# Performance work log

Measured on AMD Instinct MI355X. Metric: run time of the kernel, lower is better.

## Reference

```python
import jax, jax.numpy as jnp
import numpy as np

NEG_INF = -1e30

def mask_logits(target, mask):
    return target * mask + (1.0 - mask) * NEG_INF

def setup_inputs() -> dict:
    key = jax.random.key(0)
    k1, k2, k3 = jax.random.split(key, 3)
    B, D, Lc, Lq = 32, 256, 2048, 256
    C = jax.random.normal(k1, (B, D, Lc), dtype=jnp.float32)
    Q = jax.random.normal(k2, (B, D, Lq), dtype=jnp.float32)
    cmask = jnp.ones((B, Lc), dtype=jnp.float32)
    qmask = jnp.ones((B, Lq), dtype=jnp.float32)
    lim = np.sqrt(1.0 / D)
    w = jax.random.uniform(k3, (3 * D,), dtype=jnp.float32, minval=-lim, maxval=lim)
    return {"C": C, "Q": Q, "cmask": cmask, "qmask": qmask, "w": w}

def reference(C, Q, cmask, qmask, w):
    # C: (B, D, Lc), Q: (B, D, Lq) -> transpose to (B, L, D)
    Ct = jnp.swapaxes(C, 1, 2)            # (B, Lc, D)
    Qt = jnp.swapaxes(Q, 1, 2)            # (B, Lq, D)
    D = Ct.shape[-1]
    w1, w2, w3 = w[:D], w[D:2 * D], w[2 * D:]
    # S[b,c,q] = Ct[b,c]@w1 + Qt[b,q]@w2 + (Ct[b,c]*w3)@Qt[b,q]
    # (identical to matmul(cat([Ct,Qt,Ct*Qt],-1), w) without the 4-D tensor)
    S = (Ct @ w1)[:, :, None] + (Qt @ w2)[:, None, :] \
        + jnp.einsum('bcd,bqd->bcq', Ct * w3, Qt)     # (B, Lc, Lq)
    qm = qmask[:, None, :]                 # (B, 1, Lq)
    cm = cmask[:, :, None]                 # (B, Lc, 1)
    S1 = jax.nn.softmax(mask_logits(S, qm), axis=2)   # over query dim
    S2 = jax.nn.softmax(mask_logits(S, cm), axis=1)   # over context dim
    A = jnp.einsum('bcq,bqd->bcd', S1, Qt)            # (B, Lc, D)
    Bv = jnp.einsum('bck,bkd->bcd',
                    jnp.einsum('bcq,bkq->bck', S1, S2), Ct)  # (B, Lc, D)
    out = jnp.concatenate([Ct, A, Ct * A, Ct * Bv], axis=2)  # (B, Lc, 4D)
    # dropout omitted (eval mode)
    return jnp.swapaxes(out, 1, 2)         # (B, 4D, Lc)
```

## Files before the change

### kernel.cpp

```cpp
#include <hip/hip_runtime.h>


#define B_ 32
#define D_ 256
#define LC 2048
#define LQ 256
#define KSPLIT 4
#define NEG_INF (-1e30f)

using bf16   = __bf16;
using bf16x4 = __attribute__((ext_vector_type(4))) __bf16;
using bf16x8 = __attribute__((ext_vector_type(8))) __bf16;
using f32x4  = __attribute__((ext_vector_type(4))) float;

static __device__ __forceinline__ f32x4 mfma16(bf16x8 a, bf16x8 b, f32x4 c) {
  return __builtin_amdgcn_mfma_f32_16x16x32_bf16(a, b, c, 0, 0, 0);
}
static __device__ __forceinline__ void nt_store4(float* p, f32x4 v) {
  __builtin_nontemporal_store(v, (f32x4*)p);
}

__global__ __launch_bounds__(256) void qprep(const float* __restrict__ Q,
                                             const float* __restrict__ w,
                                             bf16* __restrict__ Qtb,
                                             bf16* __restrict__ Qb16,
                                             float* __restrict__ bqp) {
  __shared__ float t[64][65];
  __shared__ float pb[4][64];
  const int b  = blockIdx.y;
  const int qt = (blockIdx.x >> 2) * 64;
  const int dtI = blockIdx.x & 3, dt = dtI * 64;
  const int c  = threadIdx.x & 63, r0 = threadIdx.x >> 6;
  const float* Qb = Q + (size_t)b * D_ * LQ;
  bf16* Qcb = Qb16 + (size_t)b * D_ * LQ;
  float partial = 0.f;
#pragma unroll
  for (int r = r0; r < 64; r += 4) {
    const float v = Qb[(size_t)(dt + r) * LQ + qt + c];
    t[r][c] = v;
    Qcb[(size_t)(dt + r) * LQ + qt + c] = (bf16)v;
    partial += v * w[D_ + dt + r];
  }
  pb[r0][c] = partial;
  __syncthreads();
  bf16* O = Qtb + (size_t)b * LQ * D_;
#pragma unroll
  for (int r = r0; r < 64; r += 4)
    O[(size_t)(qt + r) * D_ + dt + c] = (bf16)t[c][r];
  if (r0 == 0)
    bqp[((size_t)(b * 4 + dtI)) * LQ + qt + c] = pb[0][c] + pb[1][c] + pb[2][c] + pb[3][c];
}

__global__ __launch_bounds__(256) void k1_sgemm(
    const float* __restrict__ C, const bf16* __restrict__ Qtb,
    const float* __restrict__ w, const float* __restrict__ cmask,
    const float* __restrict__ qmask, const float* __restrict__ bqp,
    bf16* __restrict__ S1, bf16* __restrict__ S1t,
    float* __restrict__ cpmax, float* __restrict__ cpsum) {
  __shared__ union __align__(16) SmU {
    struct { bf16 As[64][72]; bf16 Bs[256][72]; } st;
    bf16 tb[256][72];
    bf16 sb[64][264];
  } smu;
  __shared__ float ared[4][64];
  __shared__ float wred[4][64];
  __shared__ float wsum[4][64];
  __shared__ float cml[64];
  __shared__ float qml[256];
  __shared__ float bql[256];

  const int b = blockIdx.y, ct = blockIdx.x, c0 = ct * 64;
  const int tid = threadIdx.x, lane = tid & 63, wv = tid >> 6;
  const float* Cb = C + (size_t)b * D_ * LC;
  const bf16* Qt = Qtb + (size_t)b * LQ * D_;
  const float* w1 = w;
  const float* w3 = w + 2 * D_;

  if (tid < 64) cml[tid] = cmask[b * LC + c0 + tid];
  qml[tid] = qmask[b * LQ + tid];
  bql[tid] = bqp[(size_t)(b * 4 + 0) * LQ + tid] + bqp[(size_t)(b * 4 + 1) * LQ + tid] +
             bqp[(size_t)(b * 4 + 2) * LQ + tid] + bqp[(size_t)(b * 4 + 3) * LQ + tid];

  f32x4 acc[4][4];
#pragma unroll
  for (int i = 0; i < 4; i++)
#pragma unroll
    for (int j = 0; j < 4; j++) acc[i][j] = {0.f, 0.f, 0.f, 0.f};
  float acc_a = 0.f;

  const int sm = tid & 63;
  const int skg = tid >> 6;

  float aPre[16];
  bf16x8 bPre[8];
#pragma unroll
  for (int i = 0; i < 16; ++i)
    aPre[i] = Cb[(size_t)(skg * 16 + i) * LC + c0 + sm];
#pragma unroll
  for (int p = 0; p < 8; ++p) {
    const int idx = (p * 256 + tid) * 8;
    bPre[p] = *(const bf16x8*)(Qt + (size_t)(idx >> 6) * D_ + (idx & 63));
  }

  for (int it = 0; it < 4; ++it) {
    const int k0 = it * 64;
#pragma unroll
    for (int i = 0; i < 16; ++i) {
      const int k = skg * 16 + i, kgl = k0 + k;
      smu.st.As[sm][k] = (bf16)(aPre[i] * w3[kgl]);
      acc_a += aPre[i] * w1[kgl];
    }
#pragma unroll
    for (int p = 0; p < 8; ++p) {
      const int idx = (p * 256 + tid) * 8;
      *(bf16x8*)(&smu.st.Bs[idx >> 6][idx & 63]) = bPre[p];
    }
    __syncthreads();
    if (it < 3) {
#pragma unroll
      for (int i = 0; i < 16; ++i)
        aPre[i] = Cb[(size_t)(k0 + 64 + skg * 16 + i) * LC + c0 + sm];
#pragma unroll
      for (int p = 0; p < 8; ++p) {
        const int idx = (p * 256 + tid) * 8;
        bPre[p] = *(const bf16x8*)(Qt + (size_t)(idx >> 6) * D_ + k0 + 64 + (idx & 63));
      }
    }
#pragma unroll
    for (int kk = 0; kk < 64; kk += 32) {
      bf16x8 af[4], bfr[4];
#pragma unroll
      for (int mi = 0; mi < 4; mi++)
        af[mi] = *(const bf16x8*)(&smu.st.As[mi * 16 + (lane & 15)][kk + (lane >> 4) * 8]);
#pragma unroll
      for (int ni = 0; ni < 4; ni++)
        bfr[ni] = *(const bf16x8*)(&smu.st.Bs[wv * 64 + ni * 16 + (lane & 15)][kk + (lane >> 4) * 8]);
#pragma unroll
      for (int mi = 0; mi < 4; mi++)
#pragma unroll
        for (int ni = 0; ni < 4; ni++)
          acc[mi][ni] = mfma16(af[mi], bfr[ni], acc[mi][ni]);
    }
    __syncthreads();
  }

  ared[skg][sm] = acc_a;
  __syncthreads();

  const int r4 = (lane >> 4) * 4;
  const int cn = lane & 15;

#pragma unroll
  for (int mi = 0; mi < 4; mi++)
#pragma unroll
    for (int j = 0; j < 4; j++) {
      const int m = mi * 16 + r4 + j;
      const float aval = ared[0][m] + ared[1][m] + ared[2][m] + ared[3][m];
#pragma unroll
      for (int ni = 0; ni < 4; ni++) {
        const int n = wv * 64 + ni * 16 + cn;
        const bf16 sb = (bf16)(acc[mi][ni][j] + aval + bql[n]);
        acc[mi][ni][j] = (float)sb;
      }
    }

#pragma unroll
  for (int ni = 0; ni < 4; ni++) {
    const int n = wv * 64 + ni * 16 + cn;
    float mx = -3.0e38f;
#pragma unroll
    for (int mi = 0; mi < 4; mi++)
#pragma unroll
      for (int j = 0; j < 4; j++) {
        const int m = mi * 16 + r4 + j;
        const float cmv = cml[m];
        const float lg = acc[mi][ni][j] * cmv + (1.f - cmv) * NEG_INF;
        mx = fmaxf(mx, lg);
      }
    mx = fmaxf(mx, __shfl_xor(mx, 16));
    mx = fmaxf(mx, __shfl_xor(mx, 32));
    float ps = 0.f;
#pragma unroll
    for (int mi = 0; mi < 4; mi++)
#pragma unroll
      for (int j = 0; j < 4; j++) {
        const int m = mi * 16 + r4 + j;
        const float cmv = cml[m];
        const float lg = acc[mi][ni][j] * cmv + (1.f - cmv) * NEG_INF;
        ps += __expf(lg - mx);
      }
    ps += __shfl_xor(ps, 16);
    ps += __shfl_xor(ps, 32);
    if ((lane >> 4) == 0) {
      cpmax[((size_t)(b * 32 + ct)) * LQ + n] = mx;
      cpsum[((size_t)(b * 32 + ct)) * LQ + n] = ps;
    }
  }

#pragma unroll
  for (int mi = 0; mi < 4; mi++)
#pragma unroll
    for (int j = 0; j < 4; j++) {
      float mx = -3.0e38f;
#pragma unroll
      for (int ni = 0; ni < 4; ni++) {
        const int n = wv * 64 + ni * 16 + cn;
        const float qm = qml[n];
        const float lg = acc[mi][ni][j] * qm + (1.f - qm) * NEG_INF;
        mx = fmaxf(mx, lg);
      }
      for (int s = 1; s < 16; s <<= 1) mx = fmaxf(mx, __shfl_xor(mx, s));
      if (cn == 0) wred[wv][mi * 16 + r4 + j] = mx;
    }
  __syncthreads();

  float rmv[4][4];
#pragma unroll
  for (int mi = 0; mi < 4; mi++)
#pragma unroll
    for (int j = 0; j < 4; j++) {
      const int m = mi * 16 + r4 + j;
      const float rm = fmaxf(fmaxf(wred[0][m], wred[1][m]), fmaxf(wred[2][m], wred[3][m]));
      rmv[mi][j] = rm;
      float ps = 0.f;
#pragma unroll
      for (int ni = 0; ni < 4; ni++) {
        const int n = wv * 64 + ni * 16 + cn;
        const float qm = qml[n];
        const float lg = acc[mi][ni][j] * qm + (1.f - qm) * NEG_INF;
        const float e = __expf(lg - rm);
        acc[mi][ni][j] = e;
        ps += e;
      }
      for (int s = 1; s < 16; s <<= 1) ps += __shfl_xor(ps, s);
      if (cn == 0) wsum[wv][m] = ps;
    }
  __syncthreads();

#pragma unroll
  for (int mi = 0; mi < 4; mi++)
#pragma unroll
    for (int j = 0; j < 4; j++) {
      const int m = mi * 16 + r4 + j;
      const float f = cml[m] * __expf(rmv[mi][j]);
#pragma unroll
      for (int ni = 0; ni < 4; ni++) {
        const int n = wv * 64 + ni * 16 + cn;
        smu.tb[n][m] = (bf16)(acc[mi][ni][j] * f);
      }
    }
  __syncthreads();
  {
    bf16* dst = S1t + ((size_t)b * LQ + tid) * LC + c0;
#pragma unroll
    for (int jj = 0; jj < 8; ++jj)
      *(bf16x8*)(dst + jj * 8) = *(const bf16x8*)(&smu.tb[tid][jj * 8]);
  }
  __syncthreads();

#pragma unroll
  for (int mi = 0; mi < 4; mi++)
#pragma unroll
    for (int j = 0; j < 4; j++) {
      const int m = mi * 16 + r4 + j;
      const float rs = wsum[0][m] + wsum[1][m] + wsum[2][m] + wsum[3][m];
      const float rsl = 1.0f / rs;
#pragma unroll
      for (int ni = 0; ni < 4; ni++) {
        const int n = wv * 64 + ni * 16 + cn;
        smu.sb[m][n] = (bf16)(acc[mi][ni][j] * rsl);
      }
    }
  __syncthreads();
  {
    bf16* S1b = S1 + ((size_t)b * LC + c0) * LQ;
#pragma unroll
    for (int p = 0; p < 8; ++p) {
      const int flat = p * 2048 + tid * 8;
      *(bf16x8*)(S1b + flat) = *(const bf16x8*)(&smu.sb[flat >> 8][flat & 255]);
    }
  }
}

__global__ __launch_bounds__(256) void k2_colstats(const float* __restrict__ cpmax,
                                                   const float* __restrict__ cpsum,
                                                   float* __restrict__ cscl) {
  const int b = blockIdx.x, q = threadIdx.x;
  float m = -3.0e38f;
  for (int t = 0; t < 32; t++) m = fmaxf(m, cpmax[(size_t)(b * 32 + t) * LQ + q]);
  float s = 0.f;
  for (int t = 0; t < 32; t++)
    s += cpsum[(size_t)(b * 32 + t) * LQ + q] * __expf(cpmax[(size_t)(b * 32 + t) * LQ + q] - m);
  cscl[b * LQ + q] = __expf(-m) / s;
}

__global__ __launch_bounds__(256, 3) void k3_ugemm(
    const bf16* __restrict__ S1t, const float* __restrict__ C,
    float* __restrict__ Up) {
  const int g = blockIdx.x;
  const int x = g & 7, s = g >> 3;
  const int quad = (s >> 2) * 8 + x;
  const int inner = s & 3;
  const int b = quad >> 2, ks = quad & 3;
  const int qt = inner >> 1, dtI = inner & 1;
  const int mt = qt * 128, nt = dtI * 128;
  const int cbase = ks * (LC / KSPLIT);

  const int tid = threadIdx.x, lane = tid & 63, wv = tid >> 6;
  const int wm = (wv >> 1) * 64, wn = (wv & 1) * 64;
  const int fr = lane & 15, kg = lane >> 4;

  const bf16* Sb = S1t + (size_t)b * LQ * LC;
  const float* Cb = C + (size_t)b * D_ * LC;

  int qrow[4];
#pragma unroll
  for (int mi = 0; mi < 4; mi++) qrow[mi] = mt + wm + mi * 16 + fr;

  f32x4 acc[4][4];
#pragma unroll
  for (int i = 0; i < 4; i++)
#pragma unroll
    for (int j = 0; j < 4; j++) acc[i][j] = {0.f, 0.f, 0.f, 0.f};

#pragma unroll 2
  for (int k0 = 0; k0 < LC / KSPLIT; k0 += 64) {
    const int c8 = cbase + k0 + kg * 8;
    bf16x8 af[4][2];
#pragma unroll
    for (int mi = 0; mi < 4; mi++)
#pragma unroll
      for (int s2 = 0; s2 < 2; ++s2)
        af[mi][s2] = *(const bf16x8*)(Sb + (size_t)qrow[mi] * LC + c8 + s2 * 32);
    bf16x8 bfr[4][2];
#pragma unroll
    for (int ni = 0; ni < 4; ni++) {
      const float* cp = Cb + (size_t)(nt + wn + ni * 16 + fr) * LC + c8;
#pragma unroll
      for (int s2 = 0; s2 < 2; ++s2) {
        const f32x4 v0 = *(const f32x4*)(cp + s2 * 32);
        const f32x4 v1 = *(const f32x4*)(cp + s2 * 32 + 4);
        bf16x8 tt;
#pragma unroll
        for (int e = 0; e < 4; ++e) { tt[e] = (bf16)v0[e]; tt[e + 4] = (bf16)v1[e]; }
        bfr[ni][s2] = tt;
      }
    }
#pragma unroll
    for (int s2 = 0; s2 < 2; ++s2)
#pragma unroll
      for (int mi = 0; mi < 4; mi++)
#pragma unroll
        for (int ni = 0; ni < 4; ni++)
          acc[mi][ni] = mfma16(af[mi][s2], bfr[ni][s2], acc[mi][ni]);
  }

  float* Ub = Up + ((size_t)(ks * B_ + b)) * D_ * LQ;
#pragma unroll
  for (int mi = 0; mi < 4; mi++)
#pragma unroll
    for (int ni = 0; ni < 4; ni++) {
      const int q = mt + wm + mi * 16 + kg * 4;
      const int d = nt + wn + ni * 16 + fr;
      nt_store4(Ub + (size_t)d * LQ + q, acc[mi][ni]);
    }
}

__global__ __launch_bounds__(256) void k3r_reduce(const float* __restrict__ Up,
                                                  const float* __restrict__ cscl,
                                                  bf16* __restrict__ Utb) {
  const size_t NP = (size_t)B_ * D_ * LQ;
  const size_t i4 = ((size_t)blockIdx.x * 256 + threadIdx.x) * 4;
  const int b = (int)(i4 >> 16);
  const int q = (int)(i4 & (LQ - 1));
  f32x4 s = __builtin_nontemporal_load((const f32x4*)(Up + i4));
#pragma unroll
  for (int p = 1; p < KSPLIT; ++p) {
    const f32x4 v = __builtin_nontemporal_load((const f32x4*)(Up + p * NP + i4));
    s[0] += v[0]; s[1] += v[1]; s[2] += v[2]; s[3] += v[3];
  }
  const f32x4 sc = *(const f32x4*)(cscl + b * LQ + q);
  bf16x4 o = {(bf16)(s[0] * sc[0]), (bf16)(s[1] * sc[1]),
              (bf16)(s[2] * sc[2]), (bf16)(s[3] * sc[3])};
  *(bf16x4*)(Utb + i4) = o;
}

__global__ __launch_bounds__(256, 3) void k4_final(
    const bf16* __restrict__ S1, const float* __restrict__ C,
    const bf16* __restrict__ Qb16, const bf16* __restrict__ Utb,
    float* __restrict__ out) {
  __shared__ float bounce[64][131];

  const int g = blockIdx.x;
  const int x = g & 7, s = g >> 3;
  const int t = s >> 1, ntI = s & 1;
  const int pair = t * 8 + x;
  const int b = pair >> 5, ct = pair & 31;
  const int c0 = ct * 64, nt = ntI * 128;

  const int tid = threadIdx.x, lane = tid & 63, wv = tid >> 6;
  const int wm = (wv >> 1) * 32, wn = (wv & 1) * 64;
  const int fr = lane & 15, kg = lane >> 4;

  const bf16* S1b = S1 + ((size_t)b * LC + c0) * LQ;
  const float* Cb = C + (size_t)b * D_ * LC;
  const bf16* Qcb = Qb16 + (size_t)b * D_ * LQ;
  const bf16* Ub = Utb + (size_t)b * D_ * LQ;

  const int cq = (tid & 15) * 4;
  const int drb = tid >> 4;
  f32x4 creg[8];
#pragma unroll
  for (int m = 0; m < 8; ++m)
    creg[m] = *(const f32x4*)(Cb + (size_t)(nt + drb + m * 16) * LC + c0 + cq);

  f32x4 acc1[2][4], acc2[2][4];
#pragma unroll
  for (int i = 0; i < 2; i++)
#pragma unroll
    for (int j = 0; j < 4; j++) {
      acc1[i][j] = {0.f, 0.f, 0.f, 0.f};
      acc2[i][j] = {0.f, 0.f, 0.f, 0.f};
    }

#pragma unroll
  for (int k = 0; k < 8; ++k) {
    const int q8 = k * 32 + kg * 8;
    const bf16x8 af0 = *(const bf16x8*)(S1b + (size_t)(wm + fr) * LQ + q8);
    const bf16x8 af1 = *(const bf16x8*)(S1b + (size_t)(wm + 16 + fr) * LQ + q8);
#pragma unroll
    for (int ni = 0; ni < 4; ++ni) {
      const int d = nt + wn + ni * 16 + fr;
      const bf16x8 b1 = *(const bf16x8*)(Qcb + (size_t)d * LQ + q8);
      const bf16x8 b2 = *(const bf16x8*)(Ub + (size_t)d * LQ + q8);
      acc1[0][ni] = mfma16(af0, b1, acc1[0][ni]);
      acc1[1][ni] = mfma16(af1, b1, acc1[1][ni]);
      acc2[0][ni] = mfma16(af0, b2, acc2[0][ni]);
      acc2[1][ni] = mfma16(af1, b2, acc2[1][ni]);
    }
  }

  const int r4 = kg * 4;
#pragma unroll
  for (int mi = 0; mi < 2; mi++)
#pragma unroll
    for (int ni = 0; ni < 4; ni++)
#pragma unroll
      for (int j = 0; j < 4; j++)
        bounce[wm + mi * 16 + r4 + j][wn + ni * 16 + fr] = acc1[mi][ni][j];
  __syncthreads();

  const size_t outB = (size_t)b * (4 * D_) * LC;
#pragma unroll
  for (int m = 0; m < 8; ++m) {
    const int dr = drb + m * 16;
    const int d = nt + dr;
    f32x4 av;
#pragma unroll
    for (int e = 0; e < 4; ++e) av[e] = bounce[cq + e][dr];
    const f32x4 cv = creg[m];
    f32x4 ca;
#pragma unroll
    for (int e = 0; e < 4; ++e) ca[e] = cv[e] * av[e];
    nt_store4(out + outB + (size_t)d * LC + c0 + cq, cv);
    nt_store4(out + outB + (size_t)(D_ + d) * LC + c0 + cq, av);
    nt_store4(out + outB + (size_t)(2 * D_ + d) * LC + c0 + cq, ca);
  }
  __syncthreads();
#pragma unroll
  for (int mi = 0; mi < 2; mi++)
#pragma unroll
    for (int ni = 0; ni < 4; ni++)
#pragma unroll
      for (int j = 0; j < 4; j++)
        bounce[wm + mi * 16 + r4 + j][wn + ni * 16 + fr] = acc2[mi][ni][j];
  __syncthreads();
#pragma unroll
  for (int m = 0; m < 8; ++m) {
    const int dr = drb + m * 16;
    const int d = nt + dr;
    f32x4 bv;
#pragma unroll
    for (int e = 0; e < 4; ++e) bv[e] = creg[m][e] * bounce[cq + e][dr];
    nt_store4(out + outB + (size_t)(3 * D_ + d) * LC + c0 + cq, bv);
  }
}

extern "C" void kernel_launch(void* const* d_in, const int* in_sizes, int n_in,
                              void* d_out, int out_size, void* d_ws, size_t ws_size,
                              hipStream_t stream) {
  (void)in_sizes; (void)n_in; (void)out_size; (void)ws_size;
  const float* C = (const float*)d_in[0];
  const float* Q = (const float*)d_in[1];
  const float* cmask = (const float*)d_in[2];
  const float* qmask = (const float*)d_in[3];
  const float* w = (const float*)d_in[4];
  float* out = (float*)d_out;

  float* ws = (float*)d_ws;
  float* Up = ws;
  float* cpm = Up + (size_t)KSPLIT * B_ * D_ * LQ;
  float* cps = cpm + B_ * 32 * LQ;
  float* cscl = cps + B_ * 32 * LQ;
  float* bqp = cscl + B_ * LQ;
  bf16* S1b = (bf16*)(bqp + B_ * 4 * LQ);
  bf16* S1tb = S1b + (size_t)B_ * LC * LQ;
  bf16* Utb = S1tb + (size_t)B_ * LC * LQ;
  bf16* Qb16 = Utb + (size_t)B_ * D_ * LQ;
  bf16* Qtb = (bf16*)Up;

  qprep<<<dim3(16, B_), 256, 0, stream>>>(Q, w, Qtb, Qb16, bqp);
  k1_sgemm<<<dim3(LC / 64, B_), 256, 0, stream>>>(C, Qtb, w, cmask, qmask, bqp,
                                                  S1b, S1tb, cpm, cps);
  k2_colstats<<<dim3(B_), 256, 0, stream>>>(cpm, cps, cscl);
  k3_ugemm<<<dim3(16 * B_), 256, 0, stream>>>(S1tb, C, Up);
  k3r_reduce<<<dim3((B_ * D_ * LQ) / 1024), 256, 0, stream>>>(Up, cscl, Utb);
  k4_final<<<dim3(64 * B_), 256, 0, stream>>>(S1b, C, Qb16, Utb, out);
}
```

Measured before the change: 228.4 us.

## Double K-split in U GEMM and store bf16 partials in fragment-native layout

Raises the context-dimension split of the U GEMM from 4 to 8, doubling the grid for better occupancy, and raises the occupancy hint to 4 blocks per CU. Partial sums are now stored as bf16 in the MFMA fragment order, so the stores are contiguous and half the size of the earlier fp32 transposed stores. The reduce kernel is rewritten to read that fragment layout and map it back to (d,q) indices. This trades extra partial traffic from the larger split, plus bf16 rounding of partials, for lower bytes per partial and coalesced writes.

```diff
diff --git a/kernel.cpp b/kernel.cpp
--- a/kernel.cpp
+++ b/kernel.cpp
@@ -5,7 +5,7 @@
 #define D_ 256
 #define LC 2048
 #define LQ 256
-#define KSPLIT 4
+#define KSPLIT 8
 #define NEG_INF (-1e30f)
 
 using bf16   = __bf16;
@@ -294,14 +294,14 @@
   cscl[b * LQ + q] = __expf(-m) / s;
 }
 
-__global__ __launch_bounds__(256, 3) void k3_ugemm(
+__global__ __launch_bounds__(256, 4) void k3_ugemm(
     const bf16* __restrict__ S1t, const float* __restrict__ C,
-    float* __restrict__ Up) {
+    bf16* __restrict__ Up) {
   const int g = blockIdx.x;
   const int x = g & 7, s = g >> 3;
   const int quad = (s >> 2) * 8 + x;
   const int inner = s & 3;
-  const int b = quad >> 2, ks = quad & 3;
+  const int b = quad >> 3, ks = quad & 7;
   const int qt = inner >> 1, dtI = inner & 1;
   const int mt = qt * 128, nt = dtI * 128;
   const int cbase = ks * (LC / KSPLIT);
@@ -355,34 +355,46 @@
           acc[mi][ni] = mfma16(af[mi][s2], bfr[ni][s2], acc[mi][ni]);
   }
 
-  float* Ub = Up + ((size_t)(ks * B_ + b)) * D_ * LQ;
+  bf16* UpB = Up + ((size_t)(ks * B_ + b) * 4 + inner) * 16384;
 #pragma unroll
   for (int mi = 0; mi < 4; mi++)
 #pragma unroll
     for (int ni = 0; ni < 4; ni++) {
-      const int q = mt + wm + mi * 16 + kg * 4;
-      const int d = nt + wn + ni * 16 + fr;
-      nt_store4(Ub + (size_t)d * LQ + q, acc[mi][ni]);
-    }
-}
-
-__global__ __launch_bounds__(256) void k3r_reduce(const float* __restrict__ Up,
+      bf16x4 o = {(bf16)acc[mi][ni][0], (bf16)acc[mi][ni][1],
+                  (bf16)acc[mi][ni][2], (bf16)acc[mi][ni][3]};
+      __builtin_nontemporal_store(o, (bf16x4*)(UpB + ((mi * 4 + ni) * 256 + tid) * 4));
+    }
+}
+
+__global__ __launch_bounds__(256) void k3r_reduce(const bf16* __restrict__ Up,
                                                   const float* __restrict__ cscl,
                                                   bf16* __restrict__ Utb) {
-  const size_t NP = (size_t)B_ * D_ * LQ;
-  const size_t i4 = ((size_t)blockIdx.x * 256 + threadIdx.x) * 4;
-  const int b = (int)(i4 >> 16);
-  const int q = (int)(i4 & (LQ - 1));
-  f32x4 s = __builtin_nontemporal_load((const f32x4*)(Up + i4));
-#pragma unroll
-  for (int p = 1; p < KSPLIT; ++p) {
-    const f32x4 v = __builtin_nontemporal_load((const f32x4*)(Up + p * NP + i4));
-    s[0] += v[0]; s[1] += v[1]; s[2] += v[2]; s[3] += v[3];
+  const int g = blockIdx.x;
+  const int b = g >> 6, rest = g & 63;
+  const int inner = rest >> 4, mn = rest & 15;
+  const int mi = mn >> 2, ni = mn & 3;
+  const int qt = inner >> 1, dtI = inner & 1;
+  const int mt = qt * 128, nt = dtI * 128;
+
+  const int tid = threadIdx.x, lane = tid & 63, wv = tid >> 6;
+  const int wm = (wv >> 1) * 64, wn = (wv & 1) * 64;
+  const int fr = lane & 15, kg = lane >> 4;
+
+  const int q = mt + wm + mi * 16 + kg * 4;
+  const int d = nt + wn + ni * 16 + fr;
+  const int slot = ((mi * 4 + ni) * 256 + tid) * 4;
+
+  float s0 = 0.f, s1 = 0.f, s2 = 0.f, s3 = 0.f;
+#pragma unroll
+  for (int ks = 0; ks < KSPLIT; ++ks) {
+    const bf16x4 v = __builtin_nontemporal_load(
+        (const bf16x4*)(Up + ((size_t)(ks * B_ + b) * 4 + inner) * 16384 + slot));
+    s0 += (float)v[0]; s1 += (float)v[1]; s2 += (float)v[2]; s3 += (float)v[3];
   }
   const f32x4 sc = *(const f32x4*)(cscl + b * LQ + q);
-  bf16x4 o = {(bf16)(s[0] * sc[0]), (bf16)(s[1] * sc[1]),
-              (bf16)(s[2] * sc[2]), (bf16)(s[3] * sc[3])};
-  *(bf16x4*)(Utb + i4) = o;
+  bf16x4 o = {(bf16)(s0 * sc[0]), (bf16)(s1 * sc[1]),
+              (bf16)(s2 * sc[2]), (bf16)(s3 * sc[3])};
+  *(bf16x4*)(Utb + (size_t)b * D_ * LQ + (size_t)d * LQ + q) = o;
 }
 
 __global__ __launch_bounds__(256, 3) void k4_final(
@@ -498,8 +510,9 @@
   float* out = (float*)d_out;
 
   float* ws = (float*)d_ws;
-  float* Up = ws;
-  float* cpm = Up + (size_t)KSPLIT * B_ * D_ * LQ;
+  const size_t UPF = (size_t)4 * B_ * D_ * LQ;
+  bf16* Up = (bf16*)ws;
+  float* cpm = ws + UPF;
   float* cps = cpm + B_ * 32 * LQ;
   float* cscl = cps + B_ * 32 * LQ;
   float* bqp = cscl + B_ * LQ;
@@ -513,7 +526,7 @@
   k1_sgemm<<<dim3(LC / 64, B_), 256, 0, stream>>>(C, Qtb, w, cmask, qmask, bqp,
                                                   S1b, S1tb, cpm, cps);
   k2_colstats<<<dim3(B_), 256, 0, stream>>>(cpm, cps, cscl);
-  k3_ugemm<<<dim3(16 * B_), 256, 0, stream>>>(S1tb, C, Up);
-  k3r_reduce<<<dim3((B_ * D_ * LQ) / 1024), 256, 0, stream>>>(Up, cscl, Utb);
+  k3_ugemm<<<dim3(32 * B_), 256, 0, stream>>>(S1tb, C, Up);
+  k3r_reduce<<<dim3(64 * B_), 256, 0, stream>>>(Up, cscl, Utb);
   k4_final<<<dim3(64 * B_), 256, 0, stream>>>(S1b, C, Qb16, Utb, out);
 }
```

Result: slower. 233.2 us (+2.1%).
